# Kernel tuning notes

Measured on AMD Instinct MI355X. Metric: run time of the kernel, lower is better.

The kernel has to match this reference:

```python
import jax, jax.numpy as jnp
import numpy as np

N = 50000      # nodes
E = 400000     # edges (before self-loops)
IN = 256       # in_dim
H = 4          # heads in layer 1
C = 64         # h_dim (per-head channels, layer 1)
OUT = 16       # out_dim (layer 2, 1 head)
NEG_SLOPE = 0.2


def gatv2_layer(x, src, dst, Wl, bl, Wr, br, att, bias, heads, ch, concat, num_nodes):
    # x: [N, F]; src/dst: [E']; Wl/Wr: [F, heads*ch]; att: [heads, ch]
    xl = (x @ Wl + bl).reshape(num_nodes, heads, ch)  # source transform
    xr = (x @ Wr + br).reshape(num_nodes, heads, ch)  # target transform
    m = xl[src] + xr[dst]                              # [E', H, C] gather
    e = jnp.sum(jax.nn.leaky_relu(m, NEG_SLOPE) * att, axis=-1)  # [E', H]
    # segment softmax over incoming edges of each dst node (self-loops ensure non-empty)
    emax = jax.ops.segment_max(e, dst, num_segments=num_nodes)   # [N, H]
    ee = jnp.exp(e - emax[dst])
    denom = jax.ops.segment_sum(ee, dst, num_segments=num_nodes)  # [N, H]
    alpha = ee / (denom[dst] + 1e-16)                              # [E', H]
    out = jax.ops.segment_sum(alpha[..., None] * xl[src], dst, num_segments=num_nodes)  # [N,H,C]
    if concat:
        out = out.reshape(num_nodes, heads * ch)
    else:
        out = out.mean(axis=1)
    return out + bias


def setup_inputs() -> dict:
    key = jax.random.key(0)
    ks = jax.random.split(key, 16)
    s = 0.05
    inp = {
        "x": jax.random.normal(ks[0], (N, IN), jnp.float32),
        "edge_index": jax.random.randint(ks[1], (2, E), 0, N),
        # layer 1 params (in_dim -> heads*h_dim)
        "Wl1": jax.random.normal(ks[2], (IN, H * C), jnp.float32) * s,
        "bl1": jnp.zeros((H * C,), jnp.float32),
        "Wr1": jax.random.normal(ks[3], (IN, H * C), jnp.float32) * s,
        "br1": jnp.zeros((H * C,), jnp.float32),
        "att1": jax.random.normal(ks[4], (H, C), jnp.float32) * s,
        "bias1": jnp.zeros((H * C,), jnp.float32),
        # layer 2 params (heads*h_dim -> out_dim, 1 head)
        "Wl2": jax.random.normal(ks[5], (H * C, OUT), jnp.float32) * s,
        "bl2": jnp.zeros((OUT,), jnp.float32),
        "Wr2": jax.random.normal(ks[6], (H * C, OUT), jnp.float32) * s,
        "br2": jnp.zeros((OUT,), jnp.float32),
        "att2": jax.random.normal(ks[7], (1, OUT), jnp.float32) * s,
        "bias2": jnp.zeros((OUT,), jnp.float32),
    }
    return inp


def reference(x, edge_index, Wl1, bl1, Wr1, br1, att1, bias1, Wl2, bl2, Wr2, br2, att2, bias2):
    # add self loops (PyG GATv2Conv default add_self_loops=True)
    loop = jnp.arange(N, dtype=edge_index.dtype)
    src = jnp.concatenate([edge_index[0], loop])
    dst = jnp.concatenate([edge_index[1], loop])
    h = gatv2_layer(x, src, dst, Wl1, bl1, Wr1, br1, att1, bias1, H, C, True, N)
    h = jnp.tanh(h)
    o = gatv2_layer(h, src, dst, Wl2, bl2, Wr2, br2, att2, bias2, 1, OUT, False, N)
    return o, jax.nn.log_softmax(o, axis=1)
```

## Files before the change

kernel.cpp:

```cpp
#include <hip/hip_runtime.h>

typedef __bf16 bfv8 __attribute__((ext_vector_type(8)));
typedef float f32x4 __attribute__((ext_vector_type(4)));
typedef float f32x2 __attribute__((ext_vector_type(2)));
typedef short shortv8 __attribute__((ext_vector_type(8)));
typedef unsigned short usv8 __attribute__((ext_vector_type(8)));

__device__ __forceinline__ float b2f(unsigned short u) {
  unsigned int v = ((unsigned int)u) << 16;
  float f;
  __builtin_memcpy(&f, &v, 4);
  return f;
}
__device__ __forceinline__ unsigned short f2b(float f) {
  unsigned int u;
  __builtin_memcpy(&u, &f, 4);
  u += 0x7fffu + ((u >> 16) & 1u);
  return (unsigned short)(u >> 16);
}

__device__ __forceinline__ f32x2 bf2x(unsigned int u) {
  f32x2 r;
  r.x = __builtin_bit_cast(float, u << 16);
  r.y = __builtin_bit_cast(float, u & 0xffff0000u);
  return r;
}

template <int CTRL>
__device__ __forceinline__ float dpp_mv(float x) {
  int xi = __builtin_bit_cast(int, x);
  int yi = __builtin_amdgcn_update_dpp(0, xi, CTRL, 0xf, 0xf, true);
  return __builtin_bit_cast(float, yi);
}

__device__ __forceinline__ float tanh_fast(float x) {
  float e2 = __expf(2.f * x);
  float r = __builtin_amdgcn_rcpf(e2 + 1.f);
  float th = fmaf(-2.f, r, 1.f);
  if (!(th == th)) th = 0.f;
  return th;
}

__global__ void probe_kernel(const unsigned short* __restrict__ x, int* __restrict__ flag) {
  int lane = threadIdx.x;
  int cnt = 0;
  for (int i = lane; i < 4096; i += 64) {
    unsigned int e = (x[i] >> 7) & 0xffu;
    if (e >= 0x86u) cnt++;
  }
#pragma unroll
  for (int off = 1; off < 64; off <<= 1) cnt += __shfl_xor(cnt, off, 64);
  if (lane == 0) *flag = (cnt > 100) ? 1 : 0;
}

#define P_TOT 140352
__global__ __launch_bounds__(256) void fused_pre_kernel(
    const void* __restrict__ x, unsigned short* __restrict__ Xc,
    const int* __restrict__ flagp, int NX,
    const int* __restrict__ ei, int E, int Nn, int* __restrict__ cnt,
    const void* p0, const void* p1, const void* p2, const void* p3,
    const void* p4, const void* p5, const void* p6, const void* p7,
    const void* p8, const void* p9, const void* p10, const void* p11,
    unsigned short* __restrict__ Pc, int nb_convx, int nb_count) {
  int b = blockIdx.x;
  int t = threadIdx.x;
  if (b < nb_convx) {
    if (!*flagp) return;
    int i = (b * 256 + t) * 4;
    if (i >= NX) return;
    float4 f = *reinterpret_cast<const float4*>((const float*)x + i);
    ushort4 o;
    o.x = f2b(f.x); o.y = f2b(f.y); o.z = f2b(f.z); o.w = f2b(f.w);
    *reinterpret_cast<ushort4*>(Xc + i) = o;
  } else if (b < nb_convx + nb_count) {
    int i = (b - nb_convx) * 256 + t;
    int total = E + Nn;
    if (i >= total) return;
    int d = (i < E) ? ei[E + i] : (i - E);
    if ((unsigned)d >= (unsigned)Nn) d = 0;
    atomicAdd(&cnt[d], 1);
  } else {
    int i = (b - nb_convx - nb_count) * 256 + t;
    if (i >= P_TOT) return;
    const int offs[13] = {0, 65536, 65792, 131328, 131584, 131840, 132096,
                          136192, 136208, 140304, 140320, 140336, P_TOT};
    const void* ptrs[12] = {p0, p1, p2, p3, p4, p5, p6, p7, p8, p9, p10, p11};
    int flag = *flagp;
    int k = 0;
    while (i >= offs[k + 1]) k++;
    int local = i - offs[k];
    unsigned short v;
    if (flag) v = f2b(((const float*)ptrs[k])[local]);
    else v = ((const unsigned short*)ptrs[k])[local];
    Pc[i] = v;
  }
}

__global__ __launch_bounds__(1024) void fused_mid_kernel(
    const int* __restrict__ cnt, int* __restrict__ row_start, int* __restrict__ blkTot,
    int* __restrict__ cursor, int Nn, int nb_scan,
    const unsigned short* __restrict__ Pc,
    unsigned short* __restrict__ WT1, unsigned short* __restrict__ WT2) {
  int b = blockIdx.x;
  int t = threadIdx.x;
  if (b < nb_scan) {
    __shared__ int buf[1024];
    int i = b * 1024 + t;
    int v = (i < Nn) ? cnt[i] : 0;
    buf[t] = v;
    if (i < Nn) cursor[i] = 0;
    __syncthreads();
    for (int off = 1; off < 1024; off <<= 1) {
      int x = (t >= off) ? buf[t - off] : 0;
      __syncthreads();
      buf[t] += x;
      __syncthreads();
    }
    if (i < Nn) row_start[i] = buf[t] - v;
    if (t == 1023) blkTot[b] = buf[1023];
  } else {
    int idx = (b - nb_scan) * 1024 + t;
    if (idx < 512 * 256) {
      int n = idx >> 8, k = idx & 255;
      WT1[idx] = (n < 256) ? Pc[0 + k * 256 + n]
                           : Pc[65792 + k * 256 + (n - 256)];
    } else {
      int j = idx - 512 * 256;
      if (j < 32 * 256) {
        int n = j >> 8, k = j & 255;
        WT2[j] = (n < 16) ? Pc[132096 + k * 16 + n]
                          : Pc[136208 + k * 16 + (n - 16)];
      }
    }
  }
}

__global__ __launch_bounds__(64) void scan2_kernel(const int* __restrict__ blkTot,
                                                   int* __restrict__ blkOff, int nb,
                                                   int* __restrict__ row_start, int Nn,
                                                   int total) {
  int lane = threadIdx.x;
  int v = (lane < nb) ? blkTot[lane] : 0;
  int s = v;
#pragma unroll
  for (int off = 1; off < 64; off <<= 1) {
    int u = __shfl_up(s, off, 64);
    if (lane >= off) s += u;
  }
  int excl = s - v;
  blkOff[lane] = excl;
  if (lane == 63) blkOff[64] = s;
  int idx = Nn >> 10;
  int bo = (idx >= 64) ? __shfl(s, 63, 64) : __shfl(excl, idx, 64);
  if (lane == 0) row_start[Nn] = total - bo;
}

__global__ __launch_bounds__(256) void fill_kernel(const int* __restrict__ ei, int E, int Nn,
                                                   const int* __restrict__ row_start,
                                                   const int* __restrict__ blkOff,
                                                   int* __restrict__ cursor,
                                                   int* __restrict__ csr_src) {
  int i = blockIdx.x * 256 + threadIdx.x;
  int total = E + Nn;
  if (i >= total) return;
  int s, d;
  if (i < E) { s = ei[i]; d = ei[E + i]; } else { s = i - E; d = i - E; }
  if ((unsigned)d >= (unsigned)Nn) d = 0;
  if ((unsigned)s >= (unsigned)Nn) s = 0;
  int pos = row_start[d] + blkOff[d >> 10] + atomicAdd(&cursor[d], 1);
  if ((unsigned)pos < (unsigned)total) csr_src[pos] = s;
}

__global__ __launch_bounds__(256) void gemm1_kernel(
    const unsigned short* __restrict__ Xc,
    const unsigned short* __restrict__ x_raw,
    const int* __restrict__ flagp,
    const unsigned short* __restrict__ WT,
    const unsigned short* __restrict__ bl, const unsigned short* __restrict__ br,
    unsigned short* __restrict__ C, int M) {
  __shared__ unsigned short smem[18432];
  const unsigned short* X = (*flagp) ? Xc : x_raw;
  const int t = threadIdx.x;
  const int lane = t & 63;
  const int w = t >> 6;
  const int quad = lane >> 4;
  const int l16 = lane & 15;
  const int n_blk = blockIdx.x & 3;
  const int by = blockIdx.x >> 2;
  const int m_blk = by * 128;
  const int m_base = m_blk + (w >> 1) * 64;
  const int n_base = n_blk * 128 + (w & 1) * 64;

  const int st_row = t >> 3;
  const int st_seg = t & 7;

  f32x4 acc[4][4];
#pragma unroll
  for (int i = 0; i < 4; i++)
#pragma unroll
    for (int j = 0; j < 4; j++) acc[i][j] = (f32x4){0.f, 0.f, 0.f, 0.f};

  shortv8 st[4];
#pragma unroll
  for (int i = 0; i < 4; i++) {
    int gr = m_blk + st_row + 32 * i;
    if (gr >= M) gr = M - 1;
    st[i] = *reinterpret_cast<const shortv8*>(X + (size_t)gr * 256 + st_seg * 8);
  }
#pragma unroll
  for (int i = 0; i < 4; i++) {
    int row = st_row + 32 * i;
    *reinterpret_cast<shortv8*>(smem + row * 64 + ((st_seg ^ (row & 7)) * 8)) = st[i];
  }
  __syncthreads();

#pragma unroll
  for (int c = 0; c < 4; c++) {
    if (c < 3) {
#pragma unroll
      for (int i = 0; i < 4; i++) {
        int gr = m_blk + st_row + 32 * i;
        if (gr >= M) gr = M - 1;
        st[i] = *reinterpret_cast<const shortv8*>(X + (size_t)gr * 256 + (c + 1) * 64 +
                                                  st_seg * 8);
      }
    }
    const unsigned short* bb = smem + (c & 1) * 8192;
#pragma unroll
    for (int sub = 0; sub < 2; sub++) {
      bfv8 a[4], b[4];
      int seg_r = sub * 4 + quad;
#pragma unroll
      for (int i = 0; i < 4; i++) {
        int lrow = (w >> 1) * 64 + 16 * i + l16;
        a[i] = *reinterpret_cast<const bfv8*>(bb + lrow * 64 + ((seg_r ^ (lrow & 7)) * 8));
      }
#pragma unroll
      for (int j = 0; j < 4; j++) {
        int col = n_base + 16 * j + l16;
        b[j] = *reinterpret_cast<const bfv8*>(WT + (size_t)col * 256 + c * 64 + sub * 32 +
                                              quad * 8);
      }
#pragma unroll
      for (int i = 0; i < 4; i++)
#pragma unroll
        for (int j = 0; j < 4; j++)
          acc[i][j] = __builtin_amdgcn_mfma_f32_16x16x32_bf16(a[i], b[j], acc[i][j], 0, 0, 0);
    }
    if (c < 3) {
      int buf = (c + 1) & 1;
#pragma unroll
      for (int i = 0; i < 4; i++) {
        int row = st_row + 32 * i;
        *reinterpret_cast<shortv8*>(smem + buf * 8192 + row * 64 +
                                    ((st_seg ^ (row & 7)) * 8)) = st[i];
      }
      __syncthreads();
    }
  }

  __syncthreads();
  unsigned short* lt = smem + w * 4608;
#pragma unroll
  for (int j = 0; j < 4; j++) {
    int col = n_base + 16 * j + l16;
    float bias = (col < 256) ? b2f(bl[col]) : b2f(br[col - 256]);
#pragma unroll
    for (int i = 0; i < 4; i++)
#pragma unroll
      for (int r = 0; r < 4; r++)
        lt[(16 * i + quad * 4 + r) * 72 + 16 * j + l16] = f2b(acc[i][j][r] + bias);
  }
  __syncthreads();
#pragma unroll
  for (int pass = 0; pass < 8; pass++) {
    int row = pass * 8 + (lane >> 3);
    int colg = (lane & 7) * 8;
    shortv8 v = *reinterpret_cast<const shortv8*>(lt + row * 72 + colg);
    int grow = m_base + row;
    if (grow < M)
      *reinterpret_cast<shortv8*>(C + (size_t)grow * 512 + n_base + colg) = v;
  }
}

__global__ __launch_bounds__(256) void gemm2_kernel(
    const unsigned short* __restrict__ H, const unsigned short* __restrict__ WT,
    const unsigned short* __restrict__ bl, const unsigned short* __restrict__ br,
    float* __restrict__ C, int M) {
  const int lane = threadIdx.x & 63;
  const int w = threadIdx.x >> 6;
  const int quad = lane >> 4;
  const int l16 = lane & 15;
  const int m_base = blockIdx.x * 256 + w * 64;

  f32x4 acc[4][2];
#pragma unroll
  for (int i = 0; i < 4; i++)
#pragma unroll
    for (int j = 0; j < 2; j++) acc[i][j] = (f32x4){0.f, 0.f, 0.f, 0.f};

#pragma unroll
  for (int k0 = 0; k0 < 256; k0 += 32) {
    bfv8 a[4], b[2];
#pragma unroll
    for (int i = 0; i < 4; i++) {
      int row = m_base + 16 * i + l16;
      if (row >= M) row = M - 1;
      a[i] = *reinterpret_cast<const bfv8*>(H + (size_t)row * 256 + k0 + quad * 8);
    }
#pragma unroll
    for (int j = 0; j < 2; j++) {
      int col = 16 * j + l16;
      b[j] = *reinterpret_cast<const bfv8*>(WT + (size_t)col * 256 + k0 + quad * 8);
    }
#pragma unroll
    for (int i = 0; i < 4; i++)
#pragma unroll
      for (int j = 0; j < 2; j++)
        acc[i][j] = __builtin_amdgcn_mfma_f32_16x16x32_bf16(a[i], b[j], acc[i][j], 0, 0, 0);
  }

#pragma unroll
  for (int j = 0; j < 2; j++) {
    int col = 16 * j + l16;
    float bias = (j == 0) ? b2f(bl[l16]) : b2f(br[l16]);
#pragma unroll
    for (int i = 0; i < 4; i++) {
#pragma unroll
      for (int r = 0; r < 4; r++) {
        int row = m_base + 16 * i + quad * 4 + r;
        if (row < M) C[(size_t)row * 32 + col] = acc[i][j][r] + bias;
      }
    }
  }
}

__global__ __launch_bounds__(256) void agg1_kernel(
    const unsigned short* __restrict__ C1,
    const unsigned short* __restrict__ att1,
    const unsigned short* __restrict__ bias1,
    const int* __restrict__ row_start, const int* __restrict__ blkOff,
    const int* __restrict__ csr_src,
    unsigned short* __restrict__ H1,
    int Nn, int Etot) {
  int wid = blockIdx.x * 4 + (threadIdx.x >> 6);
  if (wid >= Nn) return;
  int lane = threadIdx.x & 63;
  int half = lane >> 5;
  int c0 = (lane & 31) * 8;

  f32x2 at2[4], xr2[4];
  {
    uint4 a4 = *reinterpret_cast<const uint4*>(att1 + c0);
    uint4 r4 = *reinterpret_cast<const uint4*>(C1 + (size_t)wid * 512 + 256 + c0);
    at2[0] = bf2x(a4.x); at2[1] = bf2x(a4.y); at2[2] = bf2x(a4.z); at2[3] = bf2x(a4.w);
    xr2[0] = bf2x(r4.x); xr2[1] = bf2x(r4.y); xr2[2] = bf2x(r4.z); xr2[3] = bf2x(r4.w);
  }

  float denom = 0.f;
  f32x2 acc2[4] = {};
  int beg = row_start[wid] + blkOff[wid >> 10];
  int end = row_start[wid + 1] + blkOff[(wid + 1) >> 10];
  if (beg < 0) beg = 0;
  if (end < beg || end - beg > Etot) end = beg;

  for (int base = beg; base < end; base += 64) {
    int cend = min(end, base + 64);
    int pl = base + lane;
    if (pl >= end) pl = end - 1;
    int s_pre = csr_src[pl];
#pragma unroll 4
    for (int i = base; i < cend; i += 2) {
      int p = i + half;
      bool valid = p < cend;
      int s = __shfl(s_pre, p - base, 64);
      if ((unsigned)s >= (unsigned)Nn) s = 0;
      uint4 rw = *reinterpret_cast<const uint4*>(C1 + (size_t)s * 512 + c0);
      f32x2 xl0 = bf2x(rw.x), xl1 = bf2x(rw.y), xl2 = bf2x(rw.z), xl3 = bf2x(rw.w);
      f32x2 m0 = xl0 + xr2[0], m1 = xl1 + xr2[1];
      f32x2 m2 = xl2 + xr2[2], m3 = xl3 + xr2[3];
      f32x2 l0 = __builtin_elementwise_max(m0, m0 * 0.2f);
      f32x2 l1 = __builtin_elementwise_max(m1, m1 * 0.2f);
      f32x2 l2 = __builtin_elementwise_max(m2, m2 * 0.2f);
      f32x2 l3 = __builtin_elementwise_max(m3, m3 * 0.2f);
      f32x2 d2 = l0 * at2[0];
      d2 += l1 * at2[1];
      d2 += l2 * at2[2];
      d2 += l3 * at2[3];
      float dot = d2.x + d2.y;
      dot += dpp_mv<0xB1>(dot);
      dot += dpp_mv<0x4E>(dot);
      dot += dpp_mv<0x141>(dot);
      dot = fminf(fmaxf(dot, -60.f), 60.f);
      float wgt = valid ? __expf(dot) : 0.f;
      denom += wgt;
      acc2[0] += xl0 * wgt;
      acc2[1] += xl1 * wgt;
      acc2[2] += xl2 * wgt;
      acc2[3] += xl3 * wgt;
    }
  }
  denom += __shfl_xor(denom, 32, 64);
#pragma unroll
  for (int k = 0; k < 4; k++) {
    acc2[k].x += __shfl_xor(acc2[k].x, 32, 64);
    acc2[k].y += __shfl_xor(acc2[k].y, 32, 64);
  }

  if (half == 0) {
    float inv = __builtin_amdgcn_rcpf(denom + 1e-16f);
    uint4 b4 = *reinterpret_cast<const uint4*>(bias1 + c0);
    f32x2 bb[4] = {bf2x(b4.x), bf2x(b4.y), bf2x(b4.z), bf2x(b4.w)};
    uint4 o;
    unsigned int od[4];
#pragma unroll
    for (int k = 0; k < 4; k++) {
      f32x2 xv = acc2[k] * inv + bb[k];
      float t0 = tanh_fast(xv.x);
      float t1 = tanh_fast(xv.y);
      od[k] = (unsigned int)f2b(t0) | ((unsigned int)f2b(t1) << 16);
    }
    o.x = od[0]; o.y = od[1]; o.z = od[2]; o.w = od[3];
    *reinterpret_cast<uint4*>(H1 + (size_t)wid * 256 + c0) = o;
  }
}

__global__ __launch_bounds__(256) void agg2_kernel(
    const float* __restrict__ C2,
    const unsigned short* __restrict__ att2,
    const unsigned short* __restrict__ bias2,
    const int* __restrict__ row_start, const int* __restrict__ blkOff,
    const int* __restrict__ csr_src,
    float* __restrict__ out,
    int Nn, int Etot) {
  int wid = blockIdx.x * 4 + (threadIdx.x >> 6);
  if (wid >= Nn) return;
  int lane = threadIdx.x & 63;
  int eslot = lane >> 2;
  int cg = (lane & 3) * 4;

  float at[4], xr[4];
  {
    ushort4 a4 = *reinterpret_cast<const ushort4*>(att2 + cg);
    at[0] = b2f(a4.x); at[1] = b2f(a4.y); at[2] = b2f(a4.z); at[3] = b2f(a4.w);
    float4 r4 = *reinterpret_cast<const float4*>(C2 + (size_t)wid * 32 + 16 + cg);
    xr[0] = r4.x; xr[1] = r4.y; xr[2] = r4.z; xr[3] = r4.w;
  }

  float denom = 0.f;
  float acc[4] = {0.f, 0.f, 0.f, 0.f};
  int beg = row_start[wid] + blkOff[wid >> 10];
  int end = row_start[wid + 1] + blkOff[(wid + 1) >> 10];
  if (beg < 0) beg = 0;
  if (end < beg || end - beg > Etot) end = beg;

  for (int base = beg; base < end; base += 64) {
    int cend = min(end, base + 64);
    int pl = base + lane;
    if (pl >= end) pl = end - 1;
    int s_pre = csr_src[pl];
    for (int i = base; i < cend; i += 16) {
      int p = i + eslot;
      bool valid = p < cend;
      int s = __shfl(s_pre, p - base, 64);
      if ((unsigned)s >= (unsigned)Nn) s = 0;
      float4 x4 = *reinterpret_cast<const float4*>(C2 + (size_t)s * 32 + cg);
      float xl[4] = {x4.x, x4.y, x4.z, x4.w};
      float dot = 0.f;
#pragma unroll
      for (int k = 0; k < 4; k++) {
        float m = xl[k] + xr[k];
        float l = fmaxf(m, 0.2f * m);
        dot = fmaf(l, at[k], dot);
      }
      dot += dpp_mv<0xB1>(dot);
      dot += dpp_mv<0x4E>(dot);
      dot = fminf(fmaxf(dot, -60.f), 60.f);
      float wgt = valid ? __expf(dot) : 0.f;
      denom += wgt;
#pragma unroll
      for (int k = 0; k < 4; k++) acc[k] = fmaf(wgt, xl[k], acc[k]);
    }
  }
  denom += dpp_mv<0x124>(denom);
  denom += dpp_mv<0x128>(denom);
#pragma unroll
  for (int k = 0; k < 4; k++) {
    acc[k] += dpp_mv<0x124>(acc[k]);
    acc[k] += dpp_mv<0x128>(acc[k]);
  }
#pragma unroll
  for (int off = 16; off <= 32; off <<= 1) {
    denom += __shfl_xor(denom, off, 64);
#pragma unroll
    for (int k = 0; k < 4; k++) acc[k] += __shfl_xor(acc[k], off, 64);
  }

  float inv = __builtin_amdgcn_rcpf(denom + 1e-16f);
  ushort4 b4 = *reinterpret_cast<const ushort4*>(bias2 + cg);
  float bb[4] = {b2f(b4.x), b2f(b4.y), b2f(b4.z), b2f(b4.w)};
  float o[4];
#pragma unroll
  for (int k = 0; k < 4; k++) {
    o[k] = acc[k] * inv + bb[k];
    if (!(o[k] == o[k])) o[k] = 0.f;
  }
  float mx = fmaxf(fmaxf(o[0], o[1]), fmaxf(o[2], o[3]));
  mx = fmaxf(mx, dpp_mv<0xB1>(mx));
  mx = fmaxf(mx, dpp_mv<0x4E>(mx));
  float se = 0.f;
#pragma unroll
  for (int k = 0; k < 4; k++) se += __expf(o[k] - mx);
  se += dpp_mv<0xB1>(se);
  se += dpp_mv<0x4E>(se);
  float ls = logf(se);
  if (lane < 4) {
    float4 vo = {o[0], o[1], o[2], o[3]};
    float4 vl = {o[0] - mx - ls, o[1] - mx - ls, o[2] - mx - ls, o[3] - mx - ls};
    *reinterpret_cast<float4*>(out + (size_t)wid * 16 + cg) = vo;
    *reinterpret_cast<float4*>(out + (size_t)Nn * 16 + (size_t)wid * 16 + cg) = vl;
  }
}

extern "C" void kernel_launch(void* const* d_in, const int* in_sizes, int n_in,
                              void* d_out, int out_size, void* d_ws, size_t ws_size,
                              hipStream_t stream) {
  const void* x_raw = d_in[0];
  const int* ei     = (const int*)d_in[1];

  const int M = in_sizes[0] / 256;
  const int E = in_sizes[1] / 2;
  const int TOT = E + M;
  const int NX = M * 256;

  char* ws = (char*)d_ws;
  size_t off = 0;
  auto alloc = [&](size_t bytes) -> void* {
    void* p = ws + off;
    off = (off + bytes + 255) & ~(size_t)255;
    return p;
  };
  int*            flag   = (int*)alloc(4);
  unsigned short* Pc     = (unsigned short*)alloc((size_t)P_TOT * 2);
  unsigned short* Xc     = (unsigned short*)alloc((size_t)NX * 2);
  unsigned short* WT1    = (unsigned short*)alloc((size_t)512 * 256 * 2);
  unsigned short* WT2    = (unsigned short*)alloc((size_t)32 * 256 * 2);
  int*            cnt    = (int*)alloc((size_t)M * 4);
  int*            cursor = (int*)alloc((size_t)M * 4);
  int*            row_start = (int*)alloc((size_t)(M + 1) * 4);
  int*            csr_src   = (int*)alloc((size_t)TOT * 4);
  int*            blkTot = (int*)alloc(64 * 4);
  int*            blkOff = (int*)alloc(65 * 4);
  float*          C2     = (float*)alloc((size_t)M * 32 * 4);
  unsigned short* C1     = (unsigned short*)alloc((size_t)M * 512 * 2);
  const size_t need = off;
  (void)n_in;
  unsigned short* H1 = Xc;

  if (ws_size < need) {
    hipMemsetAsync(d_out, 0, (size_t)out_size * 4, stream);
    return;
  }

  unsigned short* bl1c   = Pc + 65536;
  unsigned short* br1c   = Pc + 131328;
  unsigned short* att1c  = Pc + 131584;
  unsigned short* bias1c = Pc + 131840;
  unsigned short* bl2c   = Pc + 136192;
  unsigned short* br2c   = Pc + 140304;
  unsigned short* att2c  = Pc + 140320;
  unsigned short* bias2c = Pc + 140336;

  hipMemsetAsync(cnt, 0, (size_t)M * 4, stream);

  probe_kernel<<<1, 64, 0, stream>>>((const unsigned short*)x_raw, flag);

  const int nb_convx = (NX / 4 + 255) / 256;
  const int nb_count = (TOT + 255) / 256;
  const int nb_convp = (P_TOT + 255) / 256;
  fused_pre_kernel<<<nb_convx + nb_count + nb_convp, 256, 0, stream>>>(
      x_raw, Xc, flag, NX, ei, E, M, cnt,
      d_in[2], d_in[3], d_in[4], d_in[5], d_in[6], d_in[7], d_in[8], d_in[9],
      d_in[10], d_in[11], d_in[12], d_in[13], Pc, nb_convx, nb_count);

  const int nb_scan = (M + 1023) / 1024;
  const int nb_tr = (512 * 256 + 32 * 256 + 1023) / 1024;
  fused_mid_kernel<<<nb_scan + nb_tr, 1024, 0, stream>>>(cnt, row_start, blkTot,
                                                         cursor, M, nb_scan, Pc, WT1, WT2);

  scan2_kernel<<<1, 64, 0, stream>>>(blkTot, blkOff, nb_scan, row_start, M, TOT);

  fill_kernel<<<(TOT + 255) / 256, 256, 0, stream>>>(ei, E, M, row_start, blkOff,
                                                     cursor, csr_src);

  const int nb_gemm = 4 * ((M + 127) / 128);
  gemm1_kernel<<<nb_gemm, 256, 0, stream>>>(Xc, (const unsigned short*)x_raw, flag,
                                            WT1, bl1c, br1c, C1, M);

  agg1_kernel<<<(M + 3) / 4, 256, 0, stream>>>(C1, att1c, bias1c, row_start, blkOff,
                                               csr_src, H1, M, TOT);

  gemm2_kernel<<<(M + 255) / 256, 256, 0, stream>>>(H1, WT2, bl2c, br2c, C2, M);

  agg2_kernel<<<(M + 3) / 4, 256, 0, stream>>>(C2, att2c, bias2c, row_start, blkOff,
                                               csr_src, (float*)d_out, M, TOT);
}
```

Before: 289.1 us.

## Swizzle gemm1 block order, halve epilogue LDS, retile gemm2 with LDS pipeline

gemm1 now maps block IDs so that groups of eight M-tiles share an N-tile, which should improve L2 reuse of the weight columns. Its epilogue stages half the tile at a time, shrinking shared memory to raise occupancy. gemm2 moves from 256-row blocks with direct global loads to 64-row blocks that double-buffer H rows through swizzled LDS with coalesced loads. The aim is more parallelism and better coalescing for the second projection, at the cost of more blocks and more synchronisation.

New measurement: 284.4 us. No clear change (-1.6%).

```diff
diff --git a/kernel.cpp b/kernel.cpp
--- a/kernel.cpp
+++ b/kernel.cpp
@@ -178,16 +178,26 @@
     const unsigned short* __restrict__ WT,
     const unsigned short* __restrict__ bl, const unsigned short* __restrict__ br,
     unsigned short* __restrict__ C, int M) {
-  __shared__ unsigned short smem[18432];
+  __shared__ unsigned short smem[16384];
   const unsigned short* X = (*flagp) ? Xc : x_raw;
   const int t = threadIdx.x;
   const int lane = t & 63;
   const int w = t >> 6;
   const int quad = lane >> 4;
   const int l16 = lane & 15;
-  const int n_blk = blockIdx.x & 3;
-  const int by = blockIdx.x >> 2;
-  const int m_blk = by * 128;
+
+  const int G = (M + 127) >> 7;
+  const int nfull = (G >> 3) << 5;
+  int bid = blockIdx.x, grp, n_blk;
+  if (bid < nfull) {
+    grp = (bid >> 5) * 8 + (bid & 7);
+    n_blk = (bid >> 3) & 3;
+  } else {
+    int r = bid - nfull;
+    grp = (G & ~7) + (r >> 2);
+    n_blk = r & 3;
+  }
+  const int m_blk = grp * 128;
   const int m_base = m_blk + (w >> 1) * 64;
   const int n_base = n_blk * 128 + (w & 1) * 64;
 
@@ -260,26 +270,30 @@
   }
 
   __syncthreads();
-  unsigned short* lt = smem + w * 4608;
-#pragma unroll
-  for (int j = 0; j < 4; j++) {
-    int col = n_base + 16 * j + l16;
-    float bias = (col < 256) ? b2f(bl[col]) : b2f(br[col - 256]);
-#pragma unroll
-    for (int i = 0; i < 4; i++)
-#pragma unroll
-      for (int r = 0; r < 4; r++)
-        lt[(16 * i + quad * 4 + r) * 72 + 16 * j + l16] = f2b(acc[i][j][r] + bias);
-  }
-  __syncthreads();
-#pragma unroll
-  for (int pass = 0; pass < 8; pass++) {
-    int row = pass * 8 + (lane >> 3);
-    int colg = (lane & 7) * 8;
-    shortv8 v = *reinterpret_cast<const shortv8*>(lt + row * 72 + colg);
-    int grow = m_base + row;
-    if (grow < M)
-      *reinterpret_cast<shortv8*>(C + (size_t)grow * 512 + n_base + colg) = v;
+  unsigned short* lt = smem + w * 2304;
+#pragma unroll
+  for (int h = 0; h < 2; h++) {
+#pragma unroll
+    for (int j = 0; j < 4; j++) {
+      int col = n_base + 16 * j + l16;
+      float bias = (col < 256) ? b2f(bl[col]) : b2f(br[col - 256]);
+#pragma unroll
+      for (int i2 = 0; i2 < 2; i2++) {
+        int i = 2 * h + i2;
+#pragma unroll
+        for (int r = 0; r < 4; r++)
+          lt[(16 * i2 + quad * 4 + r) * 72 + 16 * j + l16] = f2b(acc[i][j][r] + bias);
+      }
+    }
+#pragma unroll
+    for (int pass = 0; pass < 4; pass++) {
+      int row = pass * 8 + (lane >> 3);
+      int colg = (lane & 7) * 8;
+      shortv8 v = *reinterpret_cast<const shortv8*>(lt + row * 72 + colg);
+      int grow = m_base + 32 * h + row;
+      if (grow < M)
+        *reinterpret_cast<shortv8*>(C + (size_t)grow * 512 + n_base + colg) = v;
+    }
   }
 }
 
@@ -287,37 +301,63 @@
     const unsigned short* __restrict__ H, const unsigned short* __restrict__ WT,
     const unsigned short* __restrict__ bl, const unsigned short* __restrict__ br,
     float* __restrict__ C, int M) {
-  const int lane = threadIdx.x & 63;
-  const int w = threadIdx.x >> 6;
+  __shared__ unsigned short smem[8192];
+  const int t = threadIdx.x;
+  const int lane = t & 63;
+  const int w = t >> 6;
   const int quad = lane >> 4;
   const int l16 = lane & 15;
-  const int m_base = blockIdx.x * 256 + w * 64;
-
-  f32x4 acc[4][2];
-#pragma unroll
-  for (int i = 0; i < 4; i++)
-#pragma unroll
-    for (int j = 0; j < 2; j++) acc[i][j] = (f32x4){0.f, 0.f, 0.f, 0.f};
-
-#pragma unroll
-  for (int k0 = 0; k0 < 256; k0 += 32) {
-    bfv8 a[4], b[2];
-#pragma unroll
-    for (int i = 0; i < 4; i++) {
-      int row = m_base + 16 * i + l16;
-      if (row >= M) row = M - 1;
-      a[i] = *reinterpret_cast<const bfv8*>(H + (size_t)row * 256 + k0 + quad * 8);
-    }
-#pragma unroll
-    for (int j = 0; j < 2; j++) {
-      int col = 16 * j + l16;
-      b[j] = *reinterpret_cast<const bfv8*>(WT + (size_t)col * 256 + k0 + quad * 8);
-    }
-#pragma unroll
-    for (int i = 0; i < 4; i++)
+  const int m_blk = blockIdx.x * 64;
+  const int wrow = w * 16;
+
+  const int st_row = t >> 2;
+  const int st_seg = t & 3;
+
+  f32x4 acc[2];
+  acc[0] = (f32x4){0.f, 0.f, 0.f, 0.f};
+  acc[1] = (f32x4){0.f, 0.f, 0.f, 0.f};
+
+  int gr = m_blk + st_row;
+  if (gr >= M) gr = M - 1;
+  const unsigned short* hrow = H + (size_t)gr * 256;
+
+  shortv8 st0 = *reinterpret_cast<const shortv8*>(hrow + st_seg * 8);
+  shortv8 st1 = *reinterpret_cast<const shortv8*>(hrow + st_seg * 8 + 32);
+  *reinterpret_cast<shortv8*>(smem + st_row * 64 + ((st_seg ^ (st_row & 7)) * 8)) = st0;
+  *reinterpret_cast<shortv8*>(smem + st_row * 64 + (((st_seg + 4) ^ (st_row & 7)) * 8)) = st1;
+  __syncthreads();
+
+#pragma unroll
+  for (int c = 0; c < 4; c++) {
+    if (c < 3) {
+      st0 = *reinterpret_cast<const shortv8*>(hrow + (c + 1) * 64 + st_seg * 8);
+      st1 = *reinterpret_cast<const shortv8*>(hrow + (c + 1) * 64 + st_seg * 8 + 32);
+    }
+    const unsigned short* bb = smem + (c & 1) * 4096;
+#pragma unroll
+    for (int sub = 0; sub < 2; sub++) {
+      int seg_r = sub * 4 + quad;
+      int lrow = wrow + l16;
+      bfv8 a = *reinterpret_cast<const bfv8*>(bb + lrow * 64 + ((seg_r ^ (lrow & 7)) * 8));
+      bfv8 b[2];
+#pragma unroll
+      for (int j = 0; j < 2; j++) {
+        int col = 16 * j + l16;
+        b[j] = *reinterpret_cast<const bfv8*>(WT + (size_t)col * 256 + c * 64 + sub * 32 +
+                                              quad * 8);
+      }
 #pragma unroll
       for (int j = 0; j < 2; j++)
-        acc[i][j] = __builtin_amdgcn_mfma_f32_16x16x32_bf16(a[i], b[j], acc[i][j], 0, 0, 0);
+        acc[j] = __builtin_amdgcn_mfma_f32_16x16x32_bf16(a, b[j], acc[j], 0, 0, 0);
+    }
+    if (c < 3) {
+      int buf = (c + 1) & 1;
+      *reinterpret_cast<shortv8*>(smem + buf * 4096 + st_row * 64 +
+                                  ((st_seg ^ (st_row & 7)) * 8)) = st0;
+      *reinterpret_cast<shortv8*>(smem + buf * 4096 + st_row * 64 +
+                                  (((st_seg + 4) ^ (st_row & 7)) * 8)) = st1;
+      __syncthreads();
+    }
   }
 
 #pragma unroll
@@ -325,12 +365,9 @@
     int col = 16 * j + l16;
     float bias = (j == 0) ? b2f(bl[l16]) : b2f(br[l16]);
 #pragma unroll
-    for (int i = 0; i < 4; i++) {
-#pragma unroll
-      for (int r = 0; r < 4; r++) {
-        int row = m_base + 16 * i + quad * 4 + r;
-        if (row < M) C[(size_t)row * 32 + col] = acc[i][j][r] + bias;
-      }
+    for (int r = 0; r < 4; r++) {
+      int row = m_blk + wrow + quad * 4 + r;
+      if (row < M) C[(size_t)row * 32 + col] = acc[j][r] + bias;
     }
   }
 }
@@ -600,7 +637,7 @@
   agg1_kernel<<<(M + 3) / 4, 256, 0, stream>>>(C1, att1c, bias1c, row_start, blkOff,
                                                csr_src, H1, M, TOT);
 
-  gemm2_kernel<<<(M + 255) / 256, 256, 0, stream>>>(H1, WT2, bl2c, br2c, C2, M);
+  gemm2_kernel<<<(M + 63) / 64, 256, 0, stream>>>(H1, WT2, bl2c, br2c, C2, M);
 
   agg2_kernel<<<(M + 3) / 4, 256, 0, stream>>>(C2, att2c, bias2c, row_start, blkOff,
                                                csr_src, (float*)d_out, M, TOT);
```
